# Kernel optimization log

Measured on AMD Instinct MI355X. Metric: run time of the kernel, lower is better.

Reference implementation:

```python
import math
import jax, jax.numpy as jnp
import numpy as np

IN_CH = 512
KEY = 512
VAL = 512
B, T = 8, 2048
SQRT_KEY = math.sqrt(float(KEY))


def setup_inputs() -> dict:
    key = jax.random.key(0)
    ks = jax.random.split(key, 7)
    s_in = 1.0 / math.sqrt(IN_CH)
    return {
        "x": jax.random.normal(ks[0], (B, T, IN_CH), dtype=jnp.float32),
        "Wq": jax.random.uniform(ks[1], (IN_CH, KEY), jnp.float32, -s_in, s_in),
        "bq": jax.random.uniform(ks[2], (KEY,), jnp.float32, -s_in, s_in),
        "Wk": jax.random.uniform(ks[3], (IN_CH, KEY), jnp.float32, -s_in, s_in),
        "bk": jax.random.uniform(ks[4], (KEY,), jnp.float32, -s_in, s_in),
        "Wv": jax.random.uniform(ks[5], (IN_CH, VAL), jnp.float32, -s_in, s_in),
        "bv": jax.random.uniform(ks[6], (VAL,), jnp.float32, -s_in, s_in),
    }


def reference(x, Wq, bq, Wk, bk, Wv, bv):
    # x: [B, T, C]
    q = x @ Wq + bq          # [B, T, K]
    k = x @ Wk + bk          # [B, T, K]
    v = x @ Wv + bv          # [B, T, V]
    logits = jnp.einsum("btk,bsk->bts", q, k)  # [B, T(q), T(kv)]
    mask = jnp.tril(jnp.ones((T, T), dtype=bool))  # causal: key s <= query t
    logits = jnp.where(mask[None, :, :], logits, -jnp.inf)
    # NOTE: original torch code softmaxes over dim=1 (the QUERY axis) — kept faithful.
    probs = jax.nn.softmax(logits / SQRT_KEY, axis=1)
    read = jnp.einsum("bts,bsv->btv", probs, v)  # [B, T, V]
    return jnp.concatenate((x, read), axis=2)    # [B, T, C+V]
```

## Files before the change

### kernel.cpp

```cpp
#include <hip/hip_runtime.h>
#include <hip/hip_bf16.h>
#include <math.h>

#define BATCH 8
#define SEQ   2048
#define CH    512
#define ROWS  (BATCH * SEQ)
#define INVSQ 0.044194173824159216f

#define TP 68

typedef __attribute__((ext_vector_type(8))) __bf16 bf16x8;
typedef __attribute__((ext_vector_type(4))) float f32x4;

__device__ inline unsigned short f2bf(float f) {
    unsigned u = __builtin_bit_cast(unsigned, f);
    u += 0x7fffu + ((u >> 16) & 1u);
    return (unsigned short)(u >> 16);
}
__device__ inline float bf2f(unsigned short s) {
    unsigned u = ((unsigned)s) << 16;
    return __builtin_bit_cast(float, u);
}

__global__ __launch_bounds__(256) void fuse_x_kernel(
    const float* __restrict__ x, unsigned short* __restrict__ xb,
    float* __restrict__ out, float* __restrict__ Z)
{
    if (blockIdx.x < 64) Z[blockIdx.x * 256 + threadIdx.x] = 0.f;
    size_t base = ((size_t)blockIdx.x * 256 + threadIdx.x) * 8;
    size_t row = base >> 9, c = base & 511;
    float4 v0 = *(const float4*)(x + base);
    float4 v1 = *(const float4*)(x + base + 4);
    float* o = out + row * 1024 + c;
    *(float4*)o = v0;
    *(float4*)(o + 4) = v1;
    alignas(16) unsigned short t[8];
    t[0] = f2bf(v0.x); t[1] = f2bf(v0.y); t[2] = f2bf(v0.z); t[3] = f2bf(v0.w);
    t[4] = f2bf(v1.x); t[5] = f2bf(v1.y); t[6] = f2bf(v1.z); t[7] = f2bf(v1.w);
    *(uint4*)(xb + base) = *(const uint4*)t;
}

__global__ __launch_bounds__(256) void transpose_w_kernel(
    const float* __restrict__ Wq, const float* __restrict__ Wk,
    const float* __restrict__ Wv, unsigned short* __restrict__ Wt)
{
    __shared__ unsigned short T[64 * TP];
    const int k0 = blockIdx.x * 64, n0 = blockIdx.y * 64, w = blockIdx.z;
    const float* W = (w == 0) ? Wq : (w == 1) ? Wk : Wv;
    const int tid = threadIdx.x;
#pragma unroll
    for (int i = 0; i < 2; ++i) {
        int slot = tid + i * 256;
        int kr = slot >> 3, c8 = (slot & 7) << 3;
        float4 a = *(const float4*)(W + (size_t)(k0 + kr) * CH + n0 + c8);
        float4 b = *(const float4*)(W + (size_t)(k0 + kr) * CH + n0 + c8 + 4);
        T[(c8 + 0) * TP + kr] = f2bf(a.x); T[(c8 + 1) * TP + kr] = f2bf(a.y);
        T[(c8 + 2) * TP + kr] = f2bf(a.z); T[(c8 + 3) * TP + kr] = f2bf(a.w);
        T[(c8 + 4) * TP + kr] = f2bf(b.x); T[(c8 + 5) * TP + kr] = f2bf(b.y);
        T[(c8 + 6) * TP + kr] = f2bf(b.z); T[(c8 + 7) * TP + kr] = f2bf(b.w);
    }
    __syncthreads();
#pragma unroll
    for (int i = 0; i < 2; ++i) {
        int slot = tid + i * 256;
        int nr = slot >> 3, k8 = (slot & 7) << 3;
        uint2 lo = *(const uint2*)(T + nr * TP + k8);
        uint2 hi = *(const uint2*)(T + nr * TP + k8 + 4);
        uint4 u; u.x = lo.x; u.y = lo.y; u.z = hi.x; u.w = hi.y;
        *(uint4*)(Wt + ((size_t)w * CH + n0 + nr) * CH + k0 + k8) = u;
    }
}

__global__ __launch_bounds__(256) void transpose_v_kernel(
    const unsigned short* __restrict__ vb, const float* __restrict__ Z,
    unsigned short* __restrict__ Vt)
{
    __shared__ unsigned short T[64 * TP];
    const int s0 = blockIdx.x * 64, v0 = blockIdx.y * 64, b = blockIdx.z;
    const int tid = threadIdx.x;
#pragma unroll
    for (int i = 0; i < 2; ++i) {
        int slot = tid + i * 256;
        int sr = slot >> 3, c8 = (slot & 7) << 3;
        float inv = 1.0f / Z[b * SEQ + s0 + sr];
        uint4 raw = *(const uint4*)(vb + ((size_t)b * SEQ + s0 + sr) * CH + v0 + c8);
        const unsigned short* p = (const unsigned short*)&raw;
#pragma unroll
        for (int j = 0; j < 8; ++j)
            T[(c8 + j) * TP + sr] = f2bf(bf2f(p[j]) * inv);
    }
    __syncthreads();
#pragma unroll
    for (int i = 0; i < 2; ++i) {
        int slot = tid + i * 256;
        int vr = slot >> 3, s8 = (slot & 7) << 3;
        uint2 lo = *(const uint2*)(T + vr * TP + s8);
        uint2 hi = *(const uint2*)(T + vr * TP + s8 + 4);
        uint4 u; u.x = lo.x; u.y = lo.y; u.z = hi.x; u.w = hi.y;
        *(uint4*)(Vt + ((size_t)b * CH + v0 + vr) * SEQ + s0 + s8) = u;
    }
}

#define STAGE4(gsrc, dslab)                                                   \
    _Pragma("unroll")                                                         \
    for (int p = 0; p < 4; ++p)                                               \
        __builtin_amdgcn_global_load_lds(                                     \
            (const __attribute__((address_space(1))) unsigned int*)((gsrc) + (size_t)p * 64 * gstride), \
            (__attribute__((address_space(3))) unsigned int*)((dslab) + p * 4096 + (tid << 3)), \
            16, 0, 0);

#define RD_A(rb)                                                              \
    a00 = *(const bf16x8*)(Ab + (arow + (rb)     * 16) * 64 + s80);           \
    a01 = *(const bf16x8*)(Ab + (arow + (rb)     * 16) * 64 + s81);           \
    a10 = *(const bf16x8*)(Ab + (arow + (rb + 1) * 16) * 64 + s80);           \
    a11 = *(const bf16x8*)(Ab + (arow + (rb + 1) * 16) * 64 + s81);

#define MFMA_PAIR(rb)                                                         \
    __builtin_amdgcn_s_setprio(1);                                            \
    _Pragma("unroll")                                                         \
    for (int cc = 0; cc < 4; ++cc)                                            \
        acc[rb][cc] = __builtin_amdgcn_mfma_f32_16x16x32_bf16(a00, b0[cc], acc[rb][cc], 0, 0, 0); \
    _Pragma("unroll")                                                         \
    for (int cc = 0; cc < 4; ++cc)                                            \
        acc[(rb) + 1][cc] = __builtin_amdgcn_mfma_f32_16x16x32_bf16(a10, b0[cc], acc[(rb) + 1][cc], 0, 0, 0); \
    _Pragma("unroll")                                                         \
    for (int cc = 0; cc < 4; ++cc)                                            \
        acc[rb][cc] = __builtin_amdgcn_mfma_f32_16x16x32_bf16(a01, b1[cc], acc[rb][cc], 0, 0, 0); \
    _Pragma("unroll")                                                         \
    for (int cc = 0; cc < 4; ++cc)                                            \
        acc[(rb) + 1][cc] = __builtin_amdgcn_mfma_f32_16x16x32_bf16(a11, b1[cc], acc[(rb) + 1][cc], 0, 0, 0); \
    __builtin_amdgcn_s_setprio(0);

#define BAR_LGKM                                                              \
    __builtin_amdgcn_s_barrier();                                             \
    asm volatile("s_waitcnt lgkmcnt(0)" ::: "memory");                        \
    __builtin_amdgcn_sched_barrier(0);

#define PIPE256(NT)                                                           \
    stageA(0); stageB(0);                                                     \
    asm volatile("s_waitcnt vmcnt(0)" ::: "memory");                          \
    __builtin_amdgcn_s_barrier();                                             \
    __builtin_amdgcn_sched_barrier(0);                                        \
    _Pragma("unroll")                                                         \
    for (int U = 0; U < (NT); ++U) {                                          \
        const unsigned short* Ab = lds + (U & 1) * 16384;                     \
        const unsigned short* Bb = lds + 32768 + (U & 1) * 16384;             \
        bf16x8 b0[4], b1[4], a00, a01, a10, a11;                              \
                                                            \
        stageA(U + 1);                                                        \
        _Pragma("unroll")                                                     \
        for (int n = 0; n < 4; ++n) {                                         \
            b0[n] = *(const bf16x8*)(Bb + (brow + n * 16) * 64 + s80);        \
            b1[n] = *(const bf16x8*)(Bb + (brow + n * 16) * 64 + s81);        \
        }                                                                     \
        RD_A(0)                                                               \
        BAR_LGKM                                                              \
        MFMA_PAIR(0)                                                          \
        __builtin_amdgcn_s_barrier();                                         \
                                                            \
        stageB(U + 1);                                                        \
        RD_A(2)                                                               \
        BAR_LGKM                                                              \
        MFMA_PAIR(2)                                                          \
        __builtin_amdgcn_s_barrier();                                         \
                                                            \
        RD_A(4)                                                               \
        BAR_LGKM                                                              \
        MFMA_PAIR(4)                                                          \
        __builtin_amdgcn_s_barrier();                                         \
                                                            \
        RD_A(6)                                                               \
        BAR_LGKM                                                              \
        MFMA_PAIR(6)                                                          \
        if (U <= (NT) - 2) asm volatile("s_waitcnt vmcnt(0)" ::: "memory");   \
        __builtin_amdgcn_s_barrier();                                         \
        __builtin_amdgcn_sched_barrier(0);                                    \
    }

__global__ __launch_bounds__(512) void qkv8_kernel(
    const unsigned short* __restrict__ xb, const unsigned short* __restrict__ Wt,
    const float* __restrict__ bq, const float* __restrict__ bk,
    const float* __restrict__ bv, unsigned short* __restrict__ qkv)
{
    __shared__ unsigned short lds[65536];
    const int tid = threadIdx.x;
    const int lane = tid & 63, wave = tid >> 6;
    const int waveA = wave >> 2;
    const int waveB = wave & 3;
    const int quad = lane >> 4, l16 = lane & 15;

    int id = (int)blockIdx.x;
    id = (id & 7) * 48 + (id >> 3);
    const int xt = id / 6, wt = id - xt * 6;
    const int xrow0 = xt << 8, wrow0 = wt << 8;

    const size_t gstride = CH;
    const unsigned short* __restrict__ Ag = Wt + (size_t)wrow0 * CH;
    const unsigned short* __restrict__ Bg = xb + (size_t)xrow0 * CH;

    const int scol = (((tid & 7) ^ ((tid >> 3) & 7)) << 3);
    const size_t ga = (size_t)(tid >> 3) * gstride + scol;
    const int s80 = ((quad ^ (l16 & 7)) << 3);
    const int s81 = s80 ^ 32;
    const int arow = waveA * 128 + l16;
    const int brow = waveB * 64 + l16;

    f32x4 acc[8][4] = {};

    auto stageA = [&](int V) {
        if (V >= 8) return;
        const unsigned short* g = Ag + ga + V * 64;
        unsigned short* d = lds + (V & 1) * 16384;
        STAGE4(g, d)
    };
    auto stageB = [&](int V) {
        if (V >= 8) return;
        const unsigned short* g = Bg + ga + V * 64;
        unsigned short* d = lds + 32768 + (V & 1) * 16384;
        STAGE4(g, d)
    };

    PIPE256(8)

    const int which = wrow0 >> 9;
    const float* bias = (which == 0) ? bq : (which == 1) ? bk : bv;
    const float scale = (which == 0) ? INVSQ : 1.0f;
    unsigned short* outw = qkv + (size_t)which * ROWS * CH;
    const int colblk = wrow0 & 511;
#pragma unroll
    for (int r = 0; r < 8; ++r) {
        int colb = colblk + waveA * 128 + r * 16 + quad * 4;
        float4 b4 = *(const float4*)(bias + colb);
#pragma unroll
        for (int c = 0; c < 4; ++c) {
            int m = xrow0 + waveB * 64 + c * 16 + l16;
            alignas(8) unsigned short pk[4];
            pk[0] = f2bf((acc[r][c][0] + b4.x) * scale);
            pk[1] = f2bf((acc[r][c][1] + b4.y) * scale);
            pk[2] = f2bf((acc[r][c][2] + b4.z) * scale);
            pk[3] = f2bf((acc[r][c][3] + b4.w) * scale);
            *(uint2*)(outw + (size_t)m * CH + colb) = *(const uint2*)pk;
        }
    }
}

__global__ __launch_bounds__(512) void logits8_kernel(
    const unsigned short* __restrict__ qb, const unsigned short* __restrict__ kb,
    unsigned short* __restrict__ E, float* __restrict__ Z)
{
    __shared__ unsigned short lds[65536];
    const int tid = threadIdx.x;
    const int lane = tid & 63, wave = tid >> 6;
    const int waveA = wave >> 2;
    const int waveB = wave & 3;
    const int quad = lane >> 4, l16 = lane & 15;

    const int b = (int)blockIdx.x & 7;
    const int i = (int)blockIdx.x >> 3;
    int tt = (int)((sqrtf(8.f * (float)i + 1.f) - 1.f) * 0.5f);
    int st = i - ((tt * (tt + 1)) >> 1);
    while (st < 0)  { --tt; st = i - ((tt * (tt + 1)) >> 1); }
    while (st > tt) { ++tt; st = i - ((tt * (tt + 1)) >> 1); }
    const int m0s = st << 8;
    const int n0t = tt << 8;

    const size_t gstride = CH;
    const unsigned short* __restrict__ Ag = kb + ((size_t)b * SEQ + m0s) * CH;
    const unsigned short* __restrict__ Bg = qb + ((size_t)b * SEQ + n0t) * CH;

    const int scol = (((tid & 7) ^ ((tid >> 3) & 7)) << 3);
    const size_t ga = (size_t)(tid >> 3) * gstride + scol;
    const int s80 = ((quad ^ (l16 & 7)) << 3);
    const int s81 = s80 ^ 32;
    const int arow = waveA * 128 + l16;
    const int brow = waveB * 64 + l16;

    f32x4 acc[8][4] = {};

    auto stageA = [&](int V) {
        if (V >= 8) return;
        const unsigned short* g = Ag + ga + V * 64;
        unsigned short* d = lds + (V & 1) * 16384;
        STAGE4(g, d)
    };
    auto stageB = [&](int V) {
        if (V >= 8) return;
        const unsigned short* g = Bg + ga + V * 64;
        unsigned short* d = lds + 32768 + (V & 1) * 16384;
        STAGE4(g, d)
    };

    PIPE256(8)

#pragma unroll
    for (int r = 0; r < 8; ++r) {
        int sb = m0s + waveA * 128 + r * 16 + quad * 4;
        float ev[4][4];
#pragma unroll
        for (int c = 0; c < 4; ++c) {
            int t = n0t + waveB * 64 + c * 16 + l16;
#pragma unroll
            for (int reg = 0; reg < 4; ++reg)
                ev[c][reg] = (sb + reg <= t) ? __expf(acc[r][c][reg]) : 0.f;
        }
#pragma unroll
        for (int reg = 0; reg < 4; ++reg) {
            float z = ev[0][reg] + ev[1][reg] + ev[2][reg] + ev[3][reg];
            z += __shfl_xor(z, 1);
            z += __shfl_xor(z, 2);
            z += __shfl_xor(z, 4);
            z += __shfl_xor(z, 8);
            if (l16 == 0) atomicAdd(&Z[b * SEQ + sb + reg], z);
        }
#pragma unroll
        for (int c = 0; c < 4; ++c) {
            int t = n0t + waveB * 64 + c * 16 + l16;
            alignas(8) unsigned short pk[4];
            pk[0] = f2bf(ev[c][0]); pk[1] = f2bf(ev[c][1]);
            pk[2] = f2bf(ev[c][2]); pk[3] = f2bf(ev[c][3]);
            *(uint2*)(E + ((size_t)b * SEQ + t) * SEQ + sb) = *(const uint2*)pk;
        }
    }
}

#define R_STAGE4(gsrc, dslab)                                                 \
    _Pragma("unroll")                                                         \
    for (int p = 0; p < 4; ++p)                                               \
        __builtin_amdgcn_global_load_lds(                                     \
            (const __attribute__((address_space(1))) unsigned int*)((gsrc) + (size_t)p * 32 * gstride), \
            (__attribute__((address_space(3))) unsigned int*)((dslab) + p * 2048 + (tid << 3)), \
            16, 0, 0);

__global__ __launch_bounds__(256, 2) void read8_kernel(
    const unsigned short* __restrict__ E, const unsigned short* __restrict__ Vt,
    float* __restrict__ out)
{
    __shared__ unsigned short lds[40960];
    const int tid = threadIdx.x;
    const int lane = tid & 63, wave = tid >> 6;
    const int waveA = wave >> 1;
    const int waveB = wave & 1;
    const int quad = lane >> 4, l16 = lane & 15;

    const int id = blockIdx.x;
    const int b = id & 7;
    const int rem = id >> 3;
    const int mv = rem & 3;
    const int r0 = rem >> 2;
    const int tt = (r0 < 8) ? r0 : 23 - r0;
    const int m0v = mv << 7;
    const int n0t = tt << 7;
    const int NT = (tt + 1) * 2;

    const size_t gstride = SEQ;
    const unsigned short* __restrict__ Ag = Vt + ((size_t)b * CH + m0v) * SEQ;
    const unsigned short* __restrict__ Bg = E + ((size_t)b * SEQ + n0t) * SEQ;

    const int scol = (((tid & 7) ^ ((tid >> 3) & 7)) << 3);
    const size_t ga = (size_t)(tid >> 3) * gstride + scol;
    const int s80 = ((quad ^ (l16 & 7)) << 3);
    const int s81 = s80 ^ 32;
    const int arow = waveA * 64 + l16;
    const int brow = waveB * 64 + l16;

    f32x4 acc[4][4] = {};

    auto stageA = [&](int V) {
        if (V >= NT) return;
        const unsigned short* g = Ag + ga + V * 64;
        unsigned short* d = lds + (V & 1) * 8192;
        R_STAGE4(g, d)
    };
    auto stageB = [&](int V) {
        if (V >= NT) return;
        const unsigned short* g = Bg + ga + V * 64;
        unsigned short* d = lds + 16384 + (V % 3) * 8192;
        R_STAGE4(g, d)
    };

    stageA(0); stageB(0); stageB(1);
    asm volatile("s_waitcnt vmcnt(4)" ::: "memory");
    __builtin_amdgcn_s_barrier();
    __builtin_amdgcn_sched_barrier(0);

#pragma unroll 2
    for (int U = 0; U < NT; ++U) {
        const unsigned short* Ab = lds + (U & 1) * 8192;
        const unsigned short* Bb = lds + 16384 + (U % 3) * 8192;
        stageA(U + 1);
        stageB(U + 2);
        bf16x8 a0[4], a1[4], c0[4], c1[4];
#pragma unroll
        for (int rr = 0; rr < 4; ++rr) {
            a0[rr] = *(const bf16x8*)(Ab + (arow + rr * 16) * 64 + s80);
            c0[rr] = *(const bf16x8*)(Bb + (brow + rr * 16) * 64 + s80);
        }
        __builtin_amdgcn_sched_barrier(0);
#pragma unroll
        for (int rr = 0; rr < 4; ++rr) {
            a1[rr] = *(const bf16x8*)(Ab + (arow + rr * 16) * 64 + s81);
            c1[rr] = *(const bf16x8*)(Bb + (brow + rr * 16) * 64 + s81);
        }
        asm volatile("s_waitcnt lgkmcnt(8)" ::: "memory");
        __builtin_amdgcn_sched_barrier(0);
        __builtin_amdgcn_s_setprio(1);
#pragma unroll
        for (int rr = 0; rr < 4; ++rr)
#pragma unroll
            for (int cc = 0; cc < 4; ++cc)
                acc[rr][cc] = __builtin_amdgcn_mfma_f32_16x16x32_bf16(
                    a0[rr], c0[cc], acc[rr][cc], 0, 0, 0);
        __builtin_amdgcn_s_setprio(0);
        asm volatile("s_waitcnt lgkmcnt(0)" ::: "memory");
        __builtin_amdgcn_sched_barrier(0);
        __builtin_amdgcn_s_setprio(1);
#pragma unroll
        for (int rr = 0; rr < 4; ++rr)
#pragma unroll
            for (int cc = 0; cc < 4; ++cc)
                acc[rr][cc] = __builtin_amdgcn_mfma_f32_16x16x32_bf16(
                    a1[rr], c1[cc], acc[rr][cc], 0, 0, 0);
        __builtin_amdgcn_s_setprio(0);
        if (U <= NT - 3)      asm volatile("s_waitcnt vmcnt(4)" ::: "memory");
        else if (U == NT - 2) asm volatile("s_waitcnt vmcnt(0)" ::: "memory");
        __builtin_amdgcn_s_barrier();
        __builtin_amdgcn_sched_barrier(0);
    }

#pragma unroll
    for (int r = 0; r < 4; ++r) {
        int v = 512 + m0v + waveA * 64 + r * 16 + quad * 4;
#pragma unroll
        for (int c = 0; c < 4; ++c) {
            int t = n0t + waveB * 64 + c * 16 + l16;
            float4 f;
            f.x = acc[r][c][0]; f.y = acc[r][c][1];
            f.z = acc[r][c][2]; f.w = acc[r][c][3];
            *(float4*)(out + ((size_t)b * SEQ + t) * 1024 + v) = f;
        }
    }
}

extern "C" void kernel_launch(void* const* d_in, const int* in_sizes, int n_in,
                              void* d_out, int out_size, void* d_ws, size_t ws_size,
                              hipStream_t stream) {
    const float* x  = (const float*)d_in[0];
    const float* Wq = (const float*)d_in[1];
    const float* bq = (const float*)d_in[2];
    const float* Wk = (const float*)d_in[3];
    const float* bk = (const float*)d_in[4];
    const float* Wv = (const float*)d_in[5];
    const float* bv = (const float*)d_in[6];
    float* out = (float*)d_out;

    char* ws = (char*)d_ws;
    const size_t QKV_BYTES = (size_t)ROWS * CH * 2;
    const size_t E_BYTES   = (size_t)BATCH * SEQ * SEQ * 2;
    unsigned short* qkv = (unsigned short*)ws;
    unsigned short* qb = qkv;
    unsigned short* kb = (unsigned short*)(ws + QKV_BYTES);
    unsigned short* vb = (unsigned short*)(ws + 2 * QKV_BYTES);
    unsigned short* E  = (unsigned short*)(ws + 3 * QKV_BYTES);
    float* Z = (float*)(ws + 3 * QKV_BYTES + E_BYTES);
    unsigned short* xb = E;
    unsigned short* Wt = (unsigned short*)((char*)E + QKV_BYTES);
    unsigned short* Vt = qb;

    dim3 blk(256);
    fuse_x_kernel<<<dim3(4096), blk, 0, stream>>>(x, xb, out, Z);
    transpose_w_kernel<<<dim3(8, 8, 3), blk, 0, stream>>>(Wq, Wk, Wv, Wt);
    qkv8_kernel<<<dim3(384), dim3(512), 0, stream>>>(xb, Wt, bq, bk, bv, qkv);
    logits8_kernel<<<dim3(288), dim3(512), 0, stream>>>(qb, kb, E, Z);
    transpose_v_kernel<<<dim3(32, 8, 8), blk, 0, stream>>>(vb, Z, Vt);
    read8_kernel<<<dim3(512), blk, 0, stream>>>(E, Vt, out);
}
```

Measured before the change: 230.7 us.

## Switch GEMM pipeline to triple-buffered K=32 stages with deeper prefetch

Both MFMA GEMM kernels (QKV projection and logits) move from a double-buffered 64-wide K slab to a triple-buffered 32-wide K slab with a new XOR swizzle. Loads are issued two stages ahead, and the wait becomes vmcnt(4) instead of vmcnt(0), so global-to-LDS copies can overlap more of the MFMA work. Total LDS use drops from 128KB to 96KB, which may allow better occupancy. The cost is twice as many loop iterations and barriers per tile, plus a more intricate wait-count scheme.

```diff
diff --git a/kernel.cpp b/kernel.cpp
--- a/kernel.cpp
+++ b/kernel.cpp
@@ -102,78 +102,63 @@
     }
 }
 
-#define STAGE4(gsrc, dslab)                                                   \
+#define STAGE2x(gsrc, dslab)                                                  \
     _Pragma("unroll")                                                         \
-    for (int p = 0; p < 4; ++p)                                               \
+    for (int j = 0; j < 2; ++j)                                               \
         __builtin_amdgcn_global_load_lds(                                     \
-            (const __attribute__((address_space(1))) unsigned int*)((gsrc) + (size_t)p * 64 * gstride), \
-            (__attribute__((address_space(3))) unsigned int*)((dslab) + p * 4096 + (tid << 3)), \
+            (const __attribute__((address_space(1))) unsigned int*)((gsrc) + (size_t)j * 128 * gstride), \
+            (__attribute__((address_space(3))) unsigned int*)((dslab) + j * 4096 + (tid << 3)), \
             16, 0, 0);
 
-#define RD_A(rb)                                                              \
-    a00 = *(const bf16x8*)(Ab + (arow + (rb)     * 16) * 64 + s80);           \
-    a01 = *(const bf16x8*)(Ab + (arow + (rb)     * 16) * 64 + s81);           \
-    a10 = *(const bf16x8*)(Ab + (arow + (rb + 1) * 16) * 64 + s80);           \
-    a11 = *(const bf16x8*)(Ab + (arow + (rb + 1) * 16) * 64 + s81);
-
-#define MFMA_PAIR(rb)                                                         \
-    __builtin_amdgcn_s_setprio(1);                                            \
-    _Pragma("unroll")                                                         \
-    for (int cc = 0; cc < 4; ++cc)                                            \
-        acc[rb][cc] = __builtin_amdgcn_mfma_f32_16x16x32_bf16(a00, b0[cc], acc[rb][cc], 0, 0, 0); \
-    _Pragma("unroll")                                                         \
-    for (int cc = 0; cc < 4; ++cc)                                            \
-        acc[(rb) + 1][cc] = __builtin_amdgcn_mfma_f32_16x16x32_bf16(a10, b0[cc], acc[(rb) + 1][cc], 0, 0, 0); \
-    _Pragma("unroll")                                                         \
-    for (int cc = 0; cc < 4; ++cc)                                            \
-        acc[rb][cc] = __builtin_amdgcn_mfma_f32_16x16x32_bf16(a01, b1[cc], acc[rb][cc], 0, 0, 0); \
-    _Pragma("unroll")                                                         \
-    for (int cc = 0; cc < 4; ++cc)                                            \
-        acc[(rb) + 1][cc] = __builtin_amdgcn_mfma_f32_16x16x32_bf16(a11, b1[cc], acc[(rb) + 1][cc], 0, 0, 0); \
-    __builtin_amdgcn_s_setprio(0);
-
-#define BAR_LGKM                                                              \
-    __builtin_amdgcn_s_barrier();                                             \
-    asm volatile("s_waitcnt lgkmcnt(0)" ::: "memory");                        \
-    __builtin_amdgcn_sched_barrier(0);
-
-#define PIPE256(NT)                                                           \
-    stageA(0); stageB(0);                                                     \
-    asm volatile("s_waitcnt vmcnt(0)" ::: "memory");                          \
+#define PIPE256_T3(NT)                                                        \
+    stageA(0); stageB(0); stageA(1); stageB(1);                               \
+    asm volatile("s_waitcnt vmcnt(4)" ::: "memory");                          \
     __builtin_amdgcn_s_barrier();                                             \
     __builtin_amdgcn_sched_barrier(0);                                        \
     _Pragma("unroll")                                                         \
     for (int U = 0; U < (NT); ++U) {                                          \
-        const unsigned short* Ab = lds + (U & 1) * 16384;                     \
-        const unsigned short* Bb = lds + 32768 + (U & 1) * 16384;             \
-        bf16x8 b0[4], b1[4], a00, a01, a10, a11;                              \
+        const unsigned short* Ab = lds + (U % 3) * 8192;                      \
+        const unsigned short* Bb = lds + 24576 + (U % 3) * 8192;              \
+        bf16x8 a[4], b[4];                                                    \
                                                             \
-        stageA(U + 1);                                                        \
+        stageA(U + 2);                                                        \
         _Pragma("unroll")                                                     \
-        for (int n = 0; n < 4; ++n) {                                         \
-            b0[n] = *(const bf16x8*)(Bb + (brow + n * 16) * 64 + s80);        \
-            b1[n] = *(const bf16x8*)(Bb + (brow + n * 16) * 64 + s81);        \
-        }                                                                     \
-        RD_A(0)                                                               \
-        BAR_LGKM                                                              \
-        MFMA_PAIR(0)                                                          \
+        for (int n = 0; n < 4; ++n)                                           \
+            b[n] = *(const bf16x8*)(Bb + (brow + n * 16) * 32 + s8w);         \
+        _Pragma("unroll")                                                     \
+        for (int r = 0; r < 4; ++r)                                           \
+            a[r] = *(const bf16x8*)(Ab + (arow + r * 16) * 32 + s8w);         \
         __builtin_amdgcn_s_barrier();                                         \
+        asm volatile("s_waitcnt lgkmcnt(0)" ::: "memory");                    \
+        __builtin_amdgcn_sched_barrier(0);                                    \
+        __builtin_amdgcn_s_setprio(1);                                        \
+        _Pragma("unroll")                                                     \
+        for (int r = 0; r < 4; ++r)                                           \
+            _Pragma("unroll")                                                 \
+            for (int c = 0; c < 4; ++c)                                       \
+                acc[r][c] = __builtin_amdgcn_mfma_f32_16x16x32_bf16(          \
+                    a[r], b[c], acc[r][c], 0, 0, 0);                          \
+        __builtin_amdgcn_s_setprio(0);                                        \
+        __builtin_amdgcn_s_barrier();                                         \
+        __builtin_amdgcn_sched_barrier(0);                                    \
                                                             \
-        stageB(U + 1);                                                        \
-        RD_A(2)                                                               \
-        BAR_LGKM                                                              \
-        MFMA_PAIR(2)                                                          \
+        stageB(U + 2);                                                        \
+        _Pragma("unroll")                                                     \
+        for (int r = 0; r < 4; ++r)                                           \
+            a[r] = *(const bf16x8*)(Ab + (arow + 64 + r * 16) * 32 + s8w);    \
         __builtin_amdgcn_s_barrier();                                         \
-                                                            \
-        RD_A(4)                                                               \
-        BAR_LGKM                                                              \
-        MFMA_PAIR(4)                                                          \
-        __builtin_amdgcn_s_barrier();                                         \
-                                                            \
-        RD_A(6)                                                               \
-        BAR_LGKM                                                              \
-        MFMA_PAIR(6)                                                          \
-        if (U <= (NT) - 2) asm volatile("s_waitcnt vmcnt(0)" ::: "memory");   \
+        asm volatile("s_waitcnt lgkmcnt(0)" ::: "memory");                    \
+        __builtin_amdgcn_sched_barrier(0);                                    \
+        __builtin_amdgcn_s_setprio(1);                                        \
+        _Pragma("unroll")                                                     \
+        for (int r = 0; r < 4; ++r)                                           \
+            _Pragma("unroll")                                                 \
+            for (int c = 0; c < 4; ++c)                                       \
+                acc[r + 4][c] = __builtin_amdgcn_mfma_f32_16x16x32_bf16(      \
+                    a[r], b[c], acc[r + 4][c], 0, 0, 0);                      \
+        __builtin_amdgcn_s_setprio(0);                                        \
+        if (U <= (NT) - 3)      asm volatile("s_waitcnt vmcnt(4)" ::: "memory"); \
+        else if (U == (NT) - 2) asm volatile("s_waitcnt vmcnt(0)" ::: "memory"); \
         __builtin_amdgcn_s_barrier();                                         \
         __builtin_amdgcn_sched_barrier(0);                                    \
     }
@@ -183,7 +168,7 @@
     const float* __restrict__ bq, const float* __restrict__ bk,
     const float* __restrict__ bv, unsigned short* __restrict__ qkv)
 {
-    __shared__ unsigned short lds[65536];
+    __shared__ unsigned short lds[49152];
     const int tid = threadIdx.x;
     const int lane = tid & 63, wave = tid >> 6;
     const int waveA = wave >> 2;
@@ -199,29 +184,28 @@
     const unsigned short* __restrict__ Ag = Wt + (size_t)wrow0 * CH;
     const unsigned short* __restrict__ Bg = xb + (size_t)xrow0 * CH;
 
-    const int scol = (((tid & 7) ^ ((tid >> 3) & 7)) << 3);
-    const size_t ga = (size_t)(tid >> 3) * gstride + scol;
-    const int s80 = ((quad ^ (l16 & 7)) << 3);
-    const int s81 = s80 ^ 32;
+    const int scol = (((tid & 3) ^ ((tid >> 4) & 3)) << 3);
+    const size_t ga = (size_t)(tid >> 2) * gstride + scol;
+    const int s8w = ((quad ^ ((l16 >> 2) & 3)) << 3);
     const int arow = waveA * 128 + l16;
     const int brow = waveB * 64 + l16;
 
     f32x4 acc[8][4] = {};
 
     auto stageA = [&](int V) {
-        if (V >= 8) return;
-        const unsigned short* g = Ag + ga + V * 64;
-        unsigned short* d = lds + (V & 1) * 16384;
-        STAGE4(g, d)
+        if (V >= 16) return;
+        const unsigned short* g = Ag + ga + V * 32;
+        unsigned short* d = lds + (V % 3) * 8192;
+        STAGE2x(g, d)
     };
     auto stageB = [&](int V) {
-        if (V >= 8) return;
-        const unsigned short* g = Bg + ga + V * 64;
-        unsigned short* d = lds + 32768 + (V & 1) * 16384;
-        STAGE4(g, d)
-    };
-
-    PIPE256(8)
+        if (V >= 16) return;
+        const unsigned short* g = Bg + ga + V * 32;
+        unsigned short* d = lds + 24576 + (V % 3) * 8192;
+        STAGE2x(g, d)
+    };
+
+    PIPE256_T3(16)
 
     const int which = wrow0 >> 9;
     const float* bias = (which == 0) ? bq : (which == 1) ? bk : bv;
@@ -249,7 +233,7 @@
     const unsigned short* __restrict__ qb, const unsigned short* __restrict__ kb,
     unsigned short* __restrict__ E, float* __restrict__ Z)
 {
-    __shared__ unsigned short lds[65536];
+    __shared__ unsigned short lds[49152];
     const int tid = threadIdx.x;
     const int lane = tid & 63, wave = tid >> 6;
     const int waveA = wave >> 2;
@@ -269,29 +253,28 @@
     const unsigned short* __restrict__ Ag = kb + ((size_t)b * SEQ + m0s) * CH;
     const unsigned short* __restrict__ Bg = qb + ((size_t)b * SEQ + n0t) * CH;
 
-    const int scol = (((tid & 7) ^ ((tid >> 3) & 7)) << 3);
-    const size_t ga = (size_t)(tid >> 3) * gstride + scol;
-    const int s80 = ((quad ^ (l16 & 7)) << 3);
-    const int s81 = s80 ^ 32;
+    const int scol = (((tid & 3) ^ ((tid >> 4) & 3)) << 3);
+    const size_t ga = (size_t)(tid >> 2) * gstride + scol;
+    const int s8w = ((quad ^ ((l16 >> 2) & 3)) << 3);
     const int arow = waveA * 128 + l16;
     const int brow = waveB * 64 + l16;
 
     f32x4 acc[8][4] = {};
 
     auto stageA = [&](int V) {
-        if (V >= 8) return;
-        const unsigned short* g = Ag + ga + V * 64;
-        unsigned short* d = lds + (V & 1) * 16384;
-        STAGE4(g, d)
+        if (V >= 16) return;
+        const unsigned short* g = Ag + ga + V * 32;
+        unsigned short* d = lds + (V % 3) * 8192;
+        STAGE2x(g, d)
     };
     auto stageB = [&](int V) {
-        if (V >= 8) return;
-        const unsigned short* g = Bg + ga + V * 64;
-        unsigned short* d = lds + 32768 + (V & 1) * 16384;
-        STAGE4(g, d)
-    };
-
-    PIPE256(8)
+        if (V >= 16) return;
+        const unsigned short* g = Bg + ga + V * 32;
+        unsigned short* d = lds + 24576 + (V % 3) * 8192;
+        STAGE2x(g, d)
+    };
+
+    PIPE256_T3(16)
 
 #pragma unroll
     for (int r = 0; r < 8; ++r) {
```

Result: slower. 239.2 us (+3.7%).

## Restage GEMM pipelines: split A loads across phases, double-buffer read kernel B

Applied to the files above, without the earlier changes.

In the QKV and logits GEMM kernels, the prefetch schedule is reordered. B is staged first and the A tile is split into two halves that are issued in separate MFMA phases, with partial vmcnt waits in place of a full drain. In the read kernel, the triple-buffered B slab becomes double-buffered, cutting LDS from 80KB to 64KB. All fragment reads now finish before a barrier, after which the next B stage is issued. This aims to spread global-to-LDS traffic and reduce stalls, at the cost of a shallower prefetch depth in the read kernel.

```diff
diff --git a/kernel.cpp b/kernel.cpp
--- a/kernel.cpp
+++ b/kernel.cpp
@@ -102,14 +102,6 @@
     }
 }
 
-#define STAGE4(gsrc, dslab)                                                   \
-    _Pragma("unroll")                                                         \
-    for (int p = 0; p < 4; ++p)                                               \
-        __builtin_amdgcn_global_load_lds(                                     \
-            (const __attribute__((address_space(1))) unsigned int*)((gsrc) + (size_t)p * 64 * gstride), \
-            (__attribute__((address_space(3))) unsigned int*)((dslab) + p * 4096 + (tid << 3)), \
-            16, 0, 0);
-
 #define RD_A(rb)                                                              \
     a00 = *(const bf16x8*)(Ab + (arow + (rb)     * 16) * 64 + s80);           \
     a01 = *(const bf16x8*)(Ab + (arow + (rb)     * 16) * 64 + s81);           \
@@ -132,14 +124,18 @@
         acc[(rb) + 1][cc] = __builtin_amdgcn_mfma_f32_16x16x32_bf16(a11, b1[cc], acc[(rb) + 1][cc], 0, 0, 0); \
     __builtin_amdgcn_s_setprio(0);
 
-#define BAR_LGKM                                                              \
+#define PH_SYNC                                                               \
     __builtin_amdgcn_s_barrier();                                             \
     asm volatile("s_waitcnt lgkmcnt(0)" ::: "memory");                        \
     __builtin_amdgcn_sched_barrier(0);
 
-#define PIPE256(NT)                                                           \
-    stageA(0); stageB(0);                                                     \
-    asm volatile("s_waitcnt vmcnt(0)" ::: "memory");                          \
+#define PH_CLOSE                                                              \
+    __builtin_amdgcn_s_barrier();                                             \
+    __builtin_amdgcn_sched_barrier(0);
+
+#define PIPE_HK(NT)                                                           \
+    stageB(0); stageAe(0); stageAl(0);                                        \
+    asm volatile("s_waitcnt vmcnt(2)" ::: "memory");                          \
     __builtin_amdgcn_s_barrier();                                             \
     __builtin_amdgcn_sched_barrier(0);                                        \
     _Pragma("unroll")                                                         \
@@ -147,36 +143,43 @@
         const unsigned short* Ab = lds + (U & 1) * 16384;                     \
         const unsigned short* Bb = lds + 32768 + (U & 1) * 16384;             \
         bf16x8 b0[4], b1[4], a00, a01, a10, a11;                              \
-                                                            \
-        stageA(U + 1);                                                        \
+                             \
+        stageB(U + 1);                                                        \
         _Pragma("unroll")                                                     \
         for (int n = 0; n < 4; ++n) {                                         \
             b0[n] = *(const bf16x8*)(Bb + (brow + n * 16) * 64 + s80);        \
             b1[n] = *(const bf16x8*)(Bb + (brow + n * 16) * 64 + s81);        \
         }                                                                     \
         RD_A(0)                                                               \
-        BAR_LGKM                                                              \
+        PH_SYNC                                                               \
         MFMA_PAIR(0)                                                          \
-        __builtin_amdgcn_s_barrier();                                         \
-                                                            \
-        stageB(U + 1);                                                        \
+        PH_CLOSE                                                              \
+                                      \
+        stageAe(U + 1);                                                       \
         RD_A(2)                                                               \
-        BAR_LGKM                                                              \
+        PH_SYNC                                                               \
         MFMA_PAIR(2)                                                          \
-        __builtin_amdgcn_s_barrier();                                         \
-                                                            \
+        if (U < (NT) - 1) asm volatile("s_waitcnt vmcnt(6)" ::: "memory");    \
+        else              asm volatile("s_waitcnt vmcnt(0)" ::: "memory");    \
+        PH_CLOSE                                                              \
+                                      \
+        stageAl(U + 1);                                                       \
         RD_A(4)                                                               \
-        BAR_LGKM                                                              \
+        PH_SYNC                                                               \
         MFMA_PAIR(4)                                                          \
-        __builtin_amdgcn_s_barrier();                                         \
-                                                            \
+        PH_CLOSE                                                              \
+                                     \
         RD_A(6)                                                               \
-        BAR_LGKM                                                              \
+        PH_SYNC                                                               \
         MFMA_PAIR(6)                                                          \
-        if (U <= (NT) - 2) asm volatile("s_waitcnt vmcnt(0)" ::: "memory");   \
-        __builtin_amdgcn_s_barrier();                                         \
-        __builtin_amdgcn_sched_barrier(0);                                    \
-    }
+        if (U < (NT) - 1) asm volatile("s_waitcnt vmcnt(2)" ::: "memory");    \
+        PH_CLOSE                                                              \
+    }
+
+#define GLD(gp, dp)                                                           \
+    __builtin_amdgcn_global_load_lds(                                         \
+        (const __attribute__((address_space(1))) unsigned int*)(gp),          \
+        (__attribute__((address_space(3))) unsigned int*)(dp), 16, 0, 0);
 
 __global__ __launch_bounds__(512) void qkv8_kernel(
     const unsigned short* __restrict__ xb, const unsigned short* __restrict__ Wt,
@@ -195,12 +198,11 @@
     const int xt = id / 6, wt = id - xt * 6;
     const int xrow0 = xt << 8, wrow0 = wt << 8;
 
-    const size_t gstride = CH;
     const unsigned short* __restrict__ Ag = Wt + (size_t)wrow0 * CH;
     const unsigned short* __restrict__ Bg = xb + (size_t)xrow0 * CH;
 
     const int scol = (((tid & 7) ^ ((tid >> 3) & 7)) << 3);
-    const size_t ga = (size_t)(tid >> 3) * gstride + scol;
+    const size_t ga = (size_t)(tid >> 3) * CH + scol;
     const int s80 = ((quad ^ (l16 & 7)) << 3);
     const int s81 = s80 ^ 32;
     const int arow = waveA * 128 + l16;
@@ -208,20 +210,29 @@
 
     f32x4 acc[8][4] = {};
 
-    auto stageA = [&](int V) {
+    auto stageB = [&](int V) {
+        if (V >= 8) return;
+        const unsigned short* g = Bg + ga + V * 64;
+        unsigned short* d = lds + 32768 + (V & 1) * 16384 + (tid << 3);
+#pragma unroll
+        for (int j = 0; j < 4; ++j) GLD(g + (size_t)j * 64 * CH, d + j * 4096)
+    };
+    auto stageAe = [&](int V) {
         if (V >= 8) return;
         const unsigned short* g = Ag + ga + V * 64;
-        unsigned short* d = lds + (V & 1) * 16384;
-        STAGE4(g, d)
-    };
-    auto stageB = [&](int V) {
-        if (V >= 8) return;
-        const unsigned short* g = Bg + ga + V * 64;
-        unsigned short* d = lds + 32768 + (V & 1) * 16384;
-        STAGE4(g, d)
-    };
-
-    PIPE256(8)
+        unsigned short* d = lds + (V & 1) * 16384 + (tid << 3);
+        GLD(g, d)
+        GLD(g + (size_t)128 * CH, d + 8192)
+    };
+    auto stageAl = [&](int V) {
+        if (V >= 8) return;
+        const unsigned short* g = Ag + ga + V * 64 + (size_t)64 * CH;
+        unsigned short* d = lds + (V & 1) * 16384 + 4096 + (tid << 3);
+        GLD(g, d)
+        GLD(g + (size_t)128 * CH, d + 8192)
+    };
+
+    PIPE_HK(8)
 
     const int which = wrow0 >> 9;
     const float* bias = (which == 0) ? bq : (which == 1) ? bk : bv;
@@ -265,12 +276,11 @@
     const int m0s = st << 8;
     const int n0t = tt << 8;
 
-    const size_t gstride = CH;
     const unsigned short* __restrict__ Ag = kb + ((size_t)b * SEQ + m0s) * CH;
     const unsigned short* __restrict__ Bg = qb + ((size_t)b * SEQ + n0t) * CH;
 
     const int scol = (((tid & 7) ^ ((tid >> 3) & 7)) << 3);
-    const size_t ga = (size_t)(tid >> 3) * gstride + scol;
+    const size_t ga = (size_t)(tid >> 3) * CH + scol;
     const int s80 = ((quad ^ (l16 & 7)) << 3);
     const int s81 = s80 ^ 32;
     const int arow = waveA * 128 + l16;
@@ -278,20 +288,29 @@
 
     f32x4 acc[8][4] = {};
 
-    auto stageA = [&](int V) {
+    auto stageB = [&](int V) {
+        if (V >= 8) return;
+        const unsigned short* g = Bg + ga + V * 64;
+        unsigned short* d = lds + 32768 + (V & 1) * 16384 + (tid << 3);
+#pragma unroll
+        for (int j = 0; j < 4; ++j) GLD(g + (size_t)j * 64 * CH, d + j * 4096)
+    };
+    auto stageAe = [&](int V) {
         if (V >= 8) return;
         const unsigned short* g = Ag + ga + V * 64;
-        unsigned short* d = lds + (V & 1) * 16384;
-        STAGE4(g, d)
-    };
-    auto stageB = [&](int V) {
-        if (V >= 8) return;
-        const unsigned short* g = Bg + ga + V * 64;
-        unsigned short* d = lds + 32768 + (V & 1) * 16384;
-        STAGE4(g, d)
-    };
-
-    PIPE256(8)
+        unsigned short* d = lds + (V & 1) * 16384 + (tid << 3);
+        GLD(g, d)
+        GLD(g + (size_t)128 * CH, d + 8192)
+    };
+    auto stageAl = [&](int V) {
+        if (V >= 8) return;
+        const unsigned short* g = Ag + ga + V * 64 + (size_t)64 * CH;
+        unsigned short* d = lds + (V & 1) * 16384 + 4096 + (tid << 3);
+        GLD(g, d)
+        GLD(g + (size_t)128 * CH, d + 8192)
+    };
+
+    PIPE_HK(8)
 
 #pragma unroll
     for (int r = 0; r < 8; ++r) {
@@ -323,20 +342,20 @@
         }
     }
 }
+#undef PIPE_HK
+#undef RD_A
+#undef MFMA_PAIR
 
 #define R_STAGE4(gsrc, dslab)                                                 \
     _Pragma("unroll")                                                         \
     for (int p = 0; p < 4; ++p)                                               \
-        __builtin_amdgcn_global_load_lds(                                     \
-            (const __attribute__((address_space(1))) unsigned int*)((gsrc) + (size_t)p * 32 * gstride), \
-            (__attribute__((address_space(3))) unsigned int*)((dslab) + p * 2048 + (tid << 3)), \
-            16, 0, 0);
+        GLD((gsrc) + (size_t)p * 32 * SEQ, (dslab) + p * 2048 + (tid << 3))
 
 __global__ __launch_bounds__(256, 2) void read8_kernel(
     const unsigned short* __restrict__ E, const unsigned short* __restrict__ Vt,
     float* __restrict__ out)
 {
-    __shared__ unsigned short lds[40960];
+    __shared__ unsigned short lds[32768];
     const int tid = threadIdx.x;
     const int lane = tid & 63, wave = tid >> 6;
     const int waveA = wave >> 1;
@@ -353,12 +372,11 @@
     const int n0t = tt << 7;
     const int NT = (tt + 1) * 2;
 
-    const size_t gstride = SEQ;
     const unsigned short* __restrict__ Ag = Vt + ((size_t)b * CH + m0v) * SEQ;
     const unsigned short* __restrict__ Bg = E + ((size_t)b * SEQ + n0t) * SEQ;
 
     const int scol = (((tid & 7) ^ ((tid >> 3) & 7)) << 3);
-    const size_t ga = (size_t)(tid >> 3) * gstride + scol;
+    const size_t ga = (size_t)(tid >> 3) * SEQ + scol;
     const int s80 = ((quad ^ (l16 & 7)) << 3);
     const int s81 = s80 ^ 32;
     const int arow = waveA * 64 + l16;
@@ -375,7 +393,7 @@
     auto stageB = [&](int V) {
         if (V >= NT) return;
         const unsigned short* g = Bg + ga + V * 64;
-        unsigned short* d = lds + 16384 + (V % 3) * 8192;
+        unsigned short* d = lds + 16384 + (V & 1) * 8192;
         R_STAGE4(g, d)
     };
 
@@ -387,23 +405,22 @@
 #pragma unroll 2
     for (int U = 0; U < NT; ++U) {
         const unsigned short* Ab = lds + (U & 1) * 8192;
-        const unsigned short* Bb = lds + 16384 + (U % 3) * 8192;
+        const unsigned short* Bb = lds + 16384 + (U & 1) * 8192;
         stageA(U + 1);
+        bf16x8 a0[4], a1[4], c0[4], c1[4];
+#pragma unroll
+        for (int rr = 0; rr < 4; ++rr) {
+            const unsigned short* ap = Ab + (arow + rr * 16) * 64;
+            const unsigned short* bp = Bb + (brow + rr * 16) * 64;
+            a0[rr] = *(const bf16x8*)(ap + s80);
+            a1[rr] = *(const bf16x8*)(ap + s81);
+            c0[rr] = *(const bf16x8*)(bp + s80);
+            c1[rr] = *(const bf16x8*)(bp + s81);
+        }
+        asm volatile("s_waitcnt lgkmcnt(0)" ::: "memory");
+        __builtin_amdgcn_s_barrier();
+        __builtin_amdgcn_sched_barrier(0);
         stageB(U + 2);
-        bf16x8 a0[4], a1[4], c0[4], c1[4];
-#pragma unroll
-        for (int rr = 0; rr < 4; ++rr) {
-            a0[rr] = *(const bf16x8*)(Ab + (arow + rr * 16) * 64 + s80);
-            c0[rr] = *(const bf16x8*)(Bb + (brow + rr * 16) * 64 + s80);
-        }
-        __builtin_amdgcn_sched_barrier(0);
-#pragma unroll
-        for (int rr = 0; rr < 4; ++rr) {
-            a1[rr] = *(const bf16x8*)(Ab + (arow + rr * 16) * 64 + s81);
-            c1[rr] = *(const bf16x8*)(Bb + (brow + rr * 16) * 64 + s81);
-        }
-        asm volatile("s_waitcnt lgkmcnt(8)" ::: "memory");
-        __builtin_amdgcn_sched_barrier(0);
         __builtin_amdgcn_s_setprio(1);
 #pragma unroll
         for (int rr = 0; rr < 4; ++rr)
@@ -411,10 +428,6 @@
             for (int cc = 0; cc < 4; ++cc)
                 acc[rr][cc] = __builtin_amdgcn_mfma_f32_16x16x32_bf16(
                     a0[rr], c0[cc], acc[rr][cc], 0, 0, 0);
-        __builtin_amdgcn_s_setprio(0);
-        asm volatile("s_waitcnt lgkmcnt(0)" ::: "memory");
-        __builtin_amdgcn_sched_barrier(0);
-        __builtin_amdgcn_s_setprio(1);
 #pragma unroll
         for (int rr = 0; rr < 4; ++rr)
 #pragma unroll
```

Measured after the change: 233.3 us. Within noise of the previous version (+1.1%).
